# Kernel tuning notes

Measured on AMD Instinct MI355X. Metric: run time of the kernel, lower is better.

## Reference

```python
import jax, jax.numpy as jnp
import numpy as np

NUM_HEADS = 16

def setup_inputs() -> dict:
    key = jax.random.key(0)
    k1, k2, k3 = jax.random.split(key, 3)
    B, N, C = 4, 2048, 1024
    x = jax.random.normal(k1, (B, N, C), dtype=jnp.float32)
    # torch Linear weights are [out_features, in_features]
    w_qkv = jax.random.normal(k2, (3 * C, C), dtype=jnp.float32) * (1.0 / np.sqrt(C))
    w_out = jax.random.normal(k3, (C, C), dtype=jnp.float32) * (1.0 / np.sqrt(C))
    b_out = jnp.zeros((C,), dtype=jnp.float32)
    return {"x": x, "w_qkv": w_qkv, "w_out": w_out, "b_out": b_out}

def reference(x, w_qkv, w_out, b_out):
    B, N, C = x.shape
    H = NUM_HEADS
    D = C // H
    scale = 1.0 / np.sqrt(D).astype(np.float32)
    # qkv projection: [B,N,3C] -> [3,B,H,N,D]
    qkv = (x @ w_qkv.T).reshape(B, N, 3, H, D).transpose(2, 0, 3, 1, 4)
    q, k, v = qkv[0], qkv[1], qkv[2]
    # The torch module's block-wise online softmax telescopes to exact softmax.
    scores = jnp.einsum("bhqd,bhkd->bhqk", q, k) * scale
    attn = jax.nn.softmax(scores, axis=-1)
    out = jnp.einsum("bhqk,bhkd->bhqd", attn, v)  # [B,H,N,D]
    out = out.transpose(0, 2, 1, 3).reshape(B, N, C)
    return out @ w_out.T + b_out
```

## Files before the change

### kernel.cpp

```cpp
#include <hip/hip_runtime.h>

typedef __attribute__((ext_vector_type(8))) short vbf8;
typedef __attribute__((ext_vector_type(4))) float vf4;

#define GLOAD16(g, l) __builtin_amdgcn_global_load_lds( \
    (const __attribute__((address_space(1))) void*)(g),  \
    (__attribute__((address_space(3))) void*)(l), 16, 0, 0)

__device__ __forceinline__ unsigned short f2bf(float f) {
  union { float f; unsigned u; } v; v.f = f;
  return (unsigned short)((v.u + 0x7fffu + ((v.u >> 16) & 1u)) >> 16);
}

__device__ __forceinline__ unsigned short cvt_bf16(float f) {
  __bf16 h = (__bf16)f;
  union { __bf16 h; unsigned short u; } v; v.h = h;
  return v.u;
}

__device__ __forceinline__ vf4 mfma16(vbf8 a, vbf8 b, vf4 c) {
  return __builtin_amdgcn_mfma_f32_16x16x32_bf16(a, b, c, 0, 0, 0);
}

__device__ __forceinline__ int swz(int row, int col) {
  return row * 64 + (col ^ ((row & 7) << 3));
}

__global__ __launch_bounds__(256)
void k_cvt_bf16(const float* __restrict__ in, unsigned short* __restrict__ out, int n4) {
  for (int i = blockIdx.x * blockDim.x + threadIdx.x; i < n4; i += gridDim.x * blockDim.x) {
    float4 v = ((const float4*)in)[i];
    ushort4 o;
    o.x = f2bf(v.x); o.y = f2bf(v.y); o.z = f2bf(v.z); o.w = f2bf(v.w);
    ((ushort4*)out)[i] = o;
  }
}

__global__ __launch_bounds__(256, 2)
void k_gemm_qkv(const unsigned short* __restrict__ A,
                const unsigned short* __restrict__ B,
                unsigned short* __restrict__ qb,
                unsigned short* __restrict__ kb,
                unsigned short* __restrict__ vtb) {
  __shared__ unsigned short As[128 * 64];
  __shared__ unsigned short Bs[128 * 64];
  const int tid = threadIdx.x;
  const int lane = tid & 63;
  const int wid = tid >> 6;
  const int wm = wid >> 1, wn = wid & 1;
  const int flat = blockIdx.y * 24 + blockIdx.x;
  const int sw = (flat & 7) * 192 + (flat >> 3);
  const int m0 = (sw / 24) * 128;
  const int n0 = (sw % 24) * 128;
  const int l15 = lane & 15, kg = lane >> 4;
  const int srow = wid * 32 + (lane >> 3);
  const int scol = (lane & 7) * 8;

  vf4 acc[4][4] = {};

  for (int kt = 0; kt < 16; ++kt) {
    __syncthreads();
    const unsigned short* gA = A + (size_t)(m0 + srow) * 1024 + kt * 64 + scol;
    const unsigned short* gB = B + (size_t)(n0 + srow) * 1024 + kt * 64 + scol;
    const unsigned ab = (unsigned)(wid * 32 * 64);
#pragma unroll
    for (int i = 0; i < 4; ++i) {
      GLOAD16(gA + (size_t)i * 8 * 1024, &As[ab + i * 8 * 64]);
      GLOAD16(gB + (size_t)i * 8 * 1024, &Bs[ab + i * 8 * 64]);
    }
    __syncthreads();
#pragma unroll
    for (int kk = 0; kk < 2; ++kk) {
      vbf8 af[4], bfr[4];
#pragma unroll
      for (int mi = 0; mi < 4; ++mi)
        af[mi] = *(const vbf8*)&As[(wm * 64 + mi * 16 + l15) * 64 + kk * 32 + kg * 8];
#pragma unroll
      for (int ni = 0; ni < 4; ++ni)
        bfr[ni] = *(const vbf8*)&Bs[(wn * 64 + ni * 16 + l15) * 64 + kk * 32 + kg * 8];
#pragma unroll
      for (int mi = 0; mi < 4; ++mi)
#pragma unroll
        for (int ni = 0; ni < 4; ++ni)
          acc[mi][ni] = mfma16(af[mi], bfr[ni], acc[mi][ni]);
    }
  }

#pragma unroll
  for (int ni = 0; ni < 4; ++ni) {
    const int c = n0 + wn * 64 + ni * 16 + l15;
    const int which = c >> 10;
    const int hd = c & 1023;
    const int h = hd >> 6, d = hd & 63;
#pragma unroll
    for (int mi = 0; mi < 4; ++mi) {
      if (which == 2) {
        const int m = m0 + wm * 64 + mi * 16 + kg * 4;
        const int b = m >> 11, nn = m & 2047;
        ushort4 pk;
        pk.x = f2bf(acc[mi][ni][0]);
        pk.y = f2bf(acc[mi][ni][1]);
        pk.z = f2bf(acc[mi][ni][2]);
        pk.w = f2bf(acc[mi][ni][3]);
        *(ushort4*)&vtb[((size_t)(b * 16 + h) * 64 + d) * 2048 + nn] = pk;
      } else {
        unsigned short* dst = (which == 0) ? qb : kb;
        const float sc = (which == 0) ? 0.18033688011112042f : 1.0f;
#pragma unroll
        for (int r = 0; r < 4; ++r) {
          const int m = m0 + wm * 64 + mi * 16 + kg * 4 + r;
          const int b = m >> 11, nn = m & 2047;
          dst[(((size_t)(b * 16 + h)) * 2048 + nn) * 64 + d] = f2bf(acc[mi][ni][r] * sc);
        }
      }
    }
  }
}

__global__ __launch_bounds__(256, 4)
void k_attn(const unsigned short* __restrict__ qb,
            const unsigned short* __restrict__ kb,
            const unsigned short* __restrict__ vt,
            unsigned short* __restrict__ ob) {
  __shared__ unsigned short Ks[2][64 * 64];
  __shared__ unsigned short Vs[64 * 64];
  __shared__ unsigned short Ps[4][32][64];
  const int tid = threadIdx.x, lane = tid & 63, w = tid >> 6;
  const int l15 = lane & 15, kg = lane >> 4;
  const int flat = blockIdx.x;
  const int sw = (flat & 7) * 128 + (flat >> 3);
  const int qt = sw & 15, bh = sw >> 4;

  const unsigned short* Q = qb + ((size_t)bh * 2048 + qt * 128 + w * 32) * 64;
  vbf8 qf[2][2];
#pragma unroll
  for (int qj = 0; qj < 2; ++qj)
#pragma unroll
    for (int kk = 0; kk < 2; ++kk)
      qf[qj][kk] = *(const vbf8*)(Q + (qj * 16 + l15) * 64 + kk * 32 + kg * 8);

  vbf8 onesv;
#pragma unroll
  for (int i = 0; i < 8; ++i) onesv[i] = (short)0x3F80;

  vf4 oacc[2][4] = {};
  vf4 lacc[2] = {};

  const int srow = lane >> 3;
  const int scol = (((lane & 7) ^ srow) * 8);
  const int pswz = (l15 & 7) << 3;
  const unsigned short* gKbase = kb + ((size_t)bh * 2048 + w * 16 + srow) * 64 + scol;
  const unsigned short* gVbase = vt + ((size_t)bh * 64 + w * 16 + srow) * 2048 + scol;

#define STAGE_K(t, b) do { \
    const unsigned short* gK_ = gKbase + (size_t)(t) * 4096; \
    GLOAD16(gK_,       &Ks[b][(w * 16) * 64]); \
    GLOAD16(gK_ + 512, &Ks[b][(w * 16 + 8) * 64]); \
  } while (0)
#define STAGE_V(t) do { \
    const unsigned short* gV_ = gVbase + (size_t)(t) * 64; \
    GLOAD16(gV_,                 &Vs[(w * 16) * 64]); \
    GLOAD16(gV_ + (size_t)16384, &Vs[(w * 16 + 8) * 64]); \
  } while (0)

  STAGE_K(0, 0);
  asm volatile("s_waitcnt vmcnt(0)" ::: "memory");
  __builtin_amdgcn_s_barrier();
  __builtin_amdgcn_sched_barrier(0);

  for (int kt = 0; kt < 32; ++kt) {
    const int cur = kt & 1;
    STAGE_V(kt);
    if (kt + 1 < 32) STAGE_K(kt + 1, cur ^ 1);

    vbf8 kfr[2][4];
#pragma unroll
    for (int kk = 0; kk < 2; ++kk)
#pragma unroll
      for (int ni = 0; ni < 4; ++ni)
        kfr[kk][ni] = *(const vbf8*)&Ks[cur][swz(ni * 16 + l15, kk * 32 + kg * 8)];

    vf4 s[2][4] = {};
    __builtin_amdgcn_s_setprio(1);
#pragma unroll
    for (int kk = 0; kk < 2; ++kk)
#pragma unroll
      for (int ni = 0; ni < 4; ++ni) {
        s[0][ni] = mfma16(kfr[kk][ni], qf[0][kk], s[0][ni]);
        s[1][ni] = mfma16(kfr[kk][ni], qf[1][kk], s[1][ni]);
      }
    __builtin_amdgcn_s_setprio(0);

#pragma unroll
    for (int qj = 0; qj < 2; ++qj)
#pragma unroll
      for (int ni = 0; ni < 4; ++ni) {
        ushort4 pk;
        pk.x = cvt_bf16(__builtin_amdgcn_exp2f(s[qj][ni][0]));
        pk.y = cvt_bf16(__builtin_amdgcn_exp2f(s[qj][ni][1]));
        pk.z = cvt_bf16(__builtin_amdgcn_exp2f(s[qj][ni][2]));
        pk.w = cvt_bf16(__builtin_amdgcn_exp2f(s[qj][ni][3]));
        *(ushort4*)&Ps[w][qj * 16 + l15][(ni * 16 + kg * 4) ^ pswz] = pk;
      }

    if (kt + 1 < 32) asm volatile("s_waitcnt vmcnt(2) lgkmcnt(0)" ::: "memory");
    else             asm volatile("s_waitcnt vmcnt(0) lgkmcnt(0)" ::: "memory");
    __builtin_amdgcn_s_barrier();
    __builtin_amdgcn_sched_barrier(0);

    __builtin_amdgcn_s_setprio(1);
#pragma unroll
    for (int kk = 0; kk < 2; ++kk) {
      const vbf8 pf0 = *(const vbf8*)&Ps[w][l15][(kk * 32 + kg * 8) ^ pswz];
      const vbf8 pf1 = *(const vbf8*)&Ps[w][16 + l15][(kk * 32 + kg * 8) ^ pswz];
      lacc[0] = mfma16(pf0, onesv, lacc[0]);
      lacc[1] = mfma16(pf1, onesv, lacc[1]);
#pragma unroll
      for (int ni = 0; ni < 4; ++ni) {
        const vbf8 vf = *(const vbf8*)&Vs[swz(ni * 16 + l15, kk * 32 + kg * 8)];
        oacc[0][ni] = mfma16(pf0, vf, oacc[0][ni]);
        oacc[1][ni] = mfma16(pf1, vf, oacc[1][ni]);
      }
    }
    __builtin_amdgcn_s_setprio(0);

    __syncthreads();
  }
#undef STAGE_K
#undef STAGE_V

  const int b = bh >> 4, h = bh & 15;
#pragma unroll
  for (int qj = 0; qj < 2; ++qj)
#pragma unroll
    for (int r = 0; r < 4; ++r) {
      const float inv = 1.0f / lacc[qj][r];
      const int q = qt * 128 + w * 32 + qj * 16 + kg * 4 + r;
#pragma unroll
      for (int ni = 0; ni < 4; ++ni)
        ob[((size_t)b * 2048 + q) * 1024 + h * 64 + ni * 16 + l15] = cvt_bf16(oacc[qj][ni][r] * inv);
    }
}

__global__ __launch_bounds__(256, 2)
void k_gemm_out(const unsigned short* __restrict__ A,
                const unsigned short* __restrict__ B,
                const float* __restrict__ bias,
                float* __restrict__ out) {
  __shared__ unsigned short As[128 * 64];
  __shared__ unsigned short Bs[128 * 64];
  const int tid = threadIdx.x;
  const int lane = tid & 63;
  const int wid = tid >> 6;
  const int wm = wid >> 1, wn = wid & 1;
  const int flat = blockIdx.y * 8 + blockIdx.x;
  const int sw = (flat & 7) * 64 + (flat >> 3);
  const int m0 = (sw / 8) * 128;
  const int n0 = (sw % 8) * 128;
  const int l15 = lane & 15, kg = lane >> 4;
  const int srow = wid * 32 + (lane >> 3);
  const int scol = (lane & 7) * 8;

  vf4 acc[4][4] = {};

  for (int kt = 0; kt < 16; ++kt) {
    __syncthreads();
    const unsigned short* gA = A + (size_t)(m0 + srow) * 1024 + kt * 64 + scol;
    const unsigned short* gB = B + (size_t)(n0 + srow) * 1024 + kt * 64 + scol;
    const unsigned ab = (unsigned)(wid * 32 * 64);
#pragma unroll
    for (int i = 0; i < 4; ++i) {
      GLOAD16(gA + (size_t)i * 8 * 1024, &As[ab + i * 8 * 64]);
      GLOAD16(gB + (size_t)i * 8 * 1024, &Bs[ab + i * 8 * 64]);
    }
    __syncthreads();
#pragma unroll
    for (int kk = 0; kk < 2; ++kk) {
      vbf8 af[4], bfr[4];
#pragma unroll
      for (int mi = 0; mi < 4; ++mi)
        af[mi] = *(const vbf8*)&As[(wm * 64 + mi * 16 + l15) * 64 + kk * 32 + kg * 8];
#pragma unroll
      for (int ni = 0; ni < 4; ++ni)
        bfr[ni] = *(const vbf8*)&Bs[(wn * 64 + ni * 16 + l15) * 64 + kk * 32 + kg * 8];
#pragma unroll
      for (int mi = 0; mi < 4; ++mi)
#pragma unroll
        for (int ni = 0; ni < 4; ++ni)
          acc[mi][ni] = mfma16(af[mi], bfr[ni], acc[mi][ni]);
    }
  }

#pragma unroll
  for (int ni = 0; ni < 4; ++ni) {
    const int c = n0 + wn * 64 + ni * 16 + l15;
    const float bv = bias[c];
#pragma unroll
    for (int mi = 0; mi < 4; ++mi) {
#pragma unroll
      for (int r = 0; r < 4; ++r) {
        const int m = m0 + wm * 64 + mi * 16 + kg * 4 + r;
        out[(size_t)m * 1024 + c] = acc[mi][ni][r] + bv;
      }
    }
  }
}

extern "C" void kernel_launch(void* const* d_in, const int* in_sizes, int n_in,
                              void* d_out, int out_size, void* d_ws, size_t ws_size,
                              hipStream_t stream) {
  const float* x     = (const float*)d_in[0];
  const float* w_qkv = (const float*)d_in[1];
  const float* w_out = (const float*)d_in[2];
  const float* b_out = (const float*)d_in[3];
  float* out = (float*)d_out;

  char* ws = (char*)d_ws;
  unsigned short* xbf   = (unsigned short*)(ws);
  unsigned short* wqkvb = (unsigned short*)(ws + 16777216);
  unsigned short* woutb = (unsigned short*)(ws + 23068672);
  unsigned short* qbuf  = (unsigned short*)(ws + 25165824);
  unsigned short* kbuf  = (unsigned short*)(ws + 41943040);
  unsigned short* vtbuf = (unsigned short*)(ws + 75497472);
  unsigned short* aob   = xbf;

  k_cvt_bf16<<<2048, 256, 0, stream>>>(x, xbf, 8388608 / 4);
  k_cvt_bf16<<<768, 256, 0, stream>>>(w_qkv, wqkvb, 3145728 / 4);
  k_cvt_bf16<<<256, 256, 0, stream>>>(w_out, woutb, 1048576 / 4);

  k_gemm_qkv<<<dim3(24, 64), 256, 0, stream>>>(xbf, wqkvb, qbuf, kbuf, vtbuf);
  k_attn<<<dim3(1024), 256, 0, stream>>>(qbuf, kbuf, vtbuf, aob);
  k_gemm_out<<<dim3(8, 64), 256, 0, stream>>>(aob, woutb, b_out, out);
}
```

Baseline: 195.2 us.

## Double-buffer V tiles and pass P via lane permutes instead of LDS

V is now double-buffered like K and prefetched one tile ahead, so each iteration waits on a single barrier instead of two syncs. The softmax probabilities P are no longer written to and read back from an LDS scratch buffer. Instead they are packed into registers and rearranged into the MFMA A-operand layout with permlane32/permlane16 swaps. This removes an LDS round-trip and a barrier per tile, at the cost of more LDS for V and higher register pressure from holding the V fragments.

```diff
diff --git a/kernel.cpp b/kernel.cpp
--- a/kernel.cpp
+++ b/kernel.cpp
@@ -2,6 +2,7 @@
 
 typedef __attribute__((ext_vector_type(8))) short vbf8;
 typedef __attribute__((ext_vector_type(4))) float vf4;
+typedef __attribute__((ext_vector_type(2))) unsigned uint2v;
 
 #define GLOAD16(g, l) __builtin_amdgcn_global_load_lds( \
     (const __attribute__((address_space(1))) void*)(g),  \
@@ -123,8 +124,7 @@
             const unsigned short* __restrict__ vt,
             unsigned short* __restrict__ ob) {
   __shared__ unsigned short Ks[2][64 * 64];
-  __shared__ unsigned short Vs[64 * 64];
-  __shared__ unsigned short Ps[4][32][64];
+  __shared__ unsigned short Vs[2][64 * 64];
   const int tid = threadIdx.x, lane = tid & 63, w = tid >> 6;
   const int l15 = lane & 15, kg = lane >> 4;
   const int flat = blockIdx.x;
@@ -148,7 +148,6 @@
 
   const int srow = lane >> 3;
   const int scol = (((lane & 7) ^ srow) * 8);
-  const int pswz = (l15 & 7) << 3;
   const unsigned short* gKbase = kb + ((size_t)bh * 2048 + w * 16 + srow) * 64 + scol;
   const unsigned short* gVbase = vt + ((size_t)bh * 64 + w * 16 + srow) * 2048 + scol;
 
@@ -157,21 +156,21 @@
     GLOAD16(gK_,       &Ks[b][(w * 16) * 64]); \
     GLOAD16(gK_ + 512, &Ks[b][(w * 16 + 8) * 64]); \
   } while (0)
-#define STAGE_V(t) do { \
+#define STAGE_V(t, b) do { \
     const unsigned short* gV_ = gVbase + (size_t)(t) * 64; \
-    GLOAD16(gV_,                 &Vs[(w * 16) * 64]); \
-    GLOAD16(gV_ + (size_t)16384, &Vs[(w * 16 + 8) * 64]); \
+    GLOAD16(gV_,                 &Vs[b][(w * 16) * 64]); \
+    GLOAD16(gV_ + (size_t)16384, &Vs[b][(w * 16 + 8) * 64]); \
   } while (0)
 
   STAGE_K(0, 0);
+  STAGE_V(0, 0);
   asm volatile("s_waitcnt vmcnt(0)" ::: "memory");
   __builtin_amdgcn_s_barrier();
   __builtin_amdgcn_sched_barrier(0);
 
   for (int kt = 0; kt < 32; ++kt) {
     const int cur = kt & 1;
-    STAGE_V(kt);
-    if (kt + 1 < 32) STAGE_K(kt + 1, cur ^ 1);
+    if (kt + 1 < 32) { STAGE_K(kt + 1, cur ^ 1); STAGE_V(kt + 1, cur ^ 1); }
 
     vbf8 kfr[2][4];
 #pragma unroll
@@ -191,40 +190,59 @@
       }
     __builtin_amdgcn_s_setprio(0);
 
+    vbf8 vfr[2][4];
+#pragma unroll
+    for (int kk = 0; kk < 2; ++kk)
+#pragma unroll
+      for (int ni = 0; ni < 4; ++ni)
+        vfr[kk][ni] = *(const vbf8*)&Vs[cur][swz(ni * 16 + l15, kk * 32 + kg * 8)];
+
+    unsigned pk[2][4][2];
 #pragma unroll
     for (int qj = 0; qj < 2; ++qj)
 #pragma unroll
       for (int ni = 0; ni < 4; ++ni) {
-        ushort4 pk;
-        pk.x = cvt_bf16(__builtin_amdgcn_exp2f(s[qj][ni][0]));
-        pk.y = cvt_bf16(__builtin_amdgcn_exp2f(s[qj][ni][1]));
-        pk.z = cvt_bf16(__builtin_amdgcn_exp2f(s[qj][ni][2]));
-        pk.w = cvt_bf16(__builtin_amdgcn_exp2f(s[qj][ni][3]));
-        *(ushort4*)&Ps[w][qj * 16 + l15][(ni * 16 + kg * 4) ^ pswz] = pk;
-      }
-
-    if (kt + 1 < 32) asm volatile("s_waitcnt vmcnt(2) lgkmcnt(0)" ::: "memory");
-    else             asm volatile("s_waitcnt vmcnt(0) lgkmcnt(0)" ::: "memory");
+        pk[qj][ni][0] = (unsigned)cvt_bf16(__builtin_amdgcn_exp2f(s[qj][ni][0]))
+                      | ((unsigned)cvt_bf16(__builtin_amdgcn_exp2f(s[qj][ni][1])) << 16);
+        pk[qj][ni][1] = (unsigned)cvt_bf16(__builtin_amdgcn_exp2f(s[qj][ni][2]))
+                      | ((unsigned)cvt_bf16(__builtin_amdgcn_exp2f(s[qj][ni][3])) << 16);
+      }
+
+    vbf8 pf[2][2];
+#pragma unroll
+    for (int qj = 0; qj < 2; ++qj)
+#pragma unroll
+      for (int n1 = 0; n1 < 2; ++n1) {
+        unsigned a0 = pk[qj][2 * n1 + 0][0], b0 = pk[qj][2 * n1 + 1][0];
+        uint2v r0 = __builtin_amdgcn_permlane32_swap(a0, b0, false, false);
+        r0 = __builtin_amdgcn_permlane16_swap(r0.x, r0.y, false, false);
+        unsigned a1 = pk[qj][2 * n1 + 0][1], b1 = pk[qj][2 * n1 + 1][1];
+        uint2v r1 = __builtin_amdgcn_permlane32_swap(a1, b1, false, false);
+        r1 = __builtin_amdgcn_permlane16_swap(r1.x, r1.y, false, false);
+        union { unsigned u[4]; vbf8 v; } U;
+        U.u[0] = r0.x;
+        U.u[1] = r1.x;
+        U.u[2] = r0.y;
+        U.u[3] = r1.y;
+        pf[qj][n1] = U.v;
+      }
+
+    __builtin_amdgcn_s_setprio(1);
+#pragma unroll
+    for (int kk = 0; kk < 2; ++kk) {
+      lacc[0] = mfma16(pf[0][kk], onesv, lacc[0]);
+      lacc[1] = mfma16(pf[1][kk], onesv, lacc[1]);
+#pragma unroll
+      for (int ni = 0; ni < 4; ++ni) {
+        oacc[0][ni] = mfma16(pf[0][kk], vfr[kk][ni], oacc[0][ni]);
+        oacc[1][ni] = mfma16(pf[1][kk], vfr[kk][ni], oacc[1][ni]);
+      }
+    }
+    __builtin_amdgcn_s_setprio(0);
+
+    asm volatile("s_waitcnt vmcnt(0)" ::: "memory");
     __builtin_amdgcn_s_barrier();
     __builtin_amdgcn_sched_barrier(0);
-
-    __builtin_amdgcn_s_setprio(1);
-#pragma unroll
-    for (int kk = 0; kk < 2; ++kk) {
-      const vbf8 pf0 = *(const vbf8*)&Ps[w][l15][(kk * 32 + kg * 8) ^ pswz];
-      const vbf8 pf1 = *(const vbf8*)&Ps[w][16 + l15][(kk * 32 + kg * 8) ^ pswz];
-      lacc[0] = mfma16(pf0, onesv, lacc[0]);
-      lacc[1] = mfma16(pf1, onesv, lacc[1]);
-#pragma unroll
-      for (int ni = 0; ni < 4; ++ni) {
-        const vbf8 vf = *(const vbf8*)&Vs[swz(ni * 16 + l15, kk * 32 + kg * 8)];
-        oacc[0][ni] = mfma16(pf0, vf, oacc[0][ni]);
-        oacc[1][ni] = mfma16(pf1, vf, oacc[1][ni]);
-      }
-    }
-    __builtin_amdgcn_s_setprio(0);
-
-    __syncthreads();
   }
 #undef STAGE_K
 #undef STAGE_V
```

After: 210.1 us. +7.6%, slower.
